# Performance work log

Hardware: AMD Instinct MI355X
Metric: run time of the kernel (lower is better)

Reference implementation:

```python
import jax, jax.numpy as jnp
from jax import lax
import numpy as np

FSIZE = 5
NUM_FILTERS = 8


def setup_inputs() -> dict:
    key = jax.random.key(0)
    k1, k2, k3 = jax.random.split(key, 3)
    B, H, W = 8, 1024, 1024
    scale = 1.0 / (FSIZE * FSIZE)  # matches .normal_(0, 1/(fsize*fsize))
    return {
        "mosaick": jax.random.uniform(k1, (B, 1, H, W), dtype=jnp.float32),
        "sel_filts": jax.random.normal(k2, (NUM_FILTERS, FSIZE, FSIZE), dtype=jnp.float32) * scale,
        "green_filts": jax.random.normal(k3, (NUM_FILTERS, FSIZE, FSIZE), dtype=jnp.float32) * scale,
    }


def _conv_bank(x_padded, filts):
    # x_padded: [B,1,H+2p,W+2p], filts: [K,f,f] -> [B,K,H,W]
    return lax.conv_general_dilated(
        x_padded, filts[:, None, :, :], (1, 1), "VALID",
        dimension_numbers=("NCHW", "OIHW", "NCHW"))


def reference(mosaick, sel_filts, green_filts):
    # Space-variant learned demosaicking of the green channel:
    # per-pixel softmax over a bank of selection-filter responses picks a
    # convex combination of candidate green interpolations; known green
    # samples (GRBG: x%2 == y%2) are passed through from the mosaick.
    B, _, H, W = mosaick.shape
    p = FSIZE // 2
    padded = jnp.pad(mosaick, ((0, 0), (0, 0), (p, p), (p, p)), mode="edge")
    sel = _conv_bank(padded, sel_filts)        # [B,K,H,W] selection scores
    interp = _conv_bank(padded, green_filts)   # [B,K,H,W] green candidates
    w = jax.nn.softmax(sel, axis=1)            # per-pixel filter weights
    green_hat = jnp.sum(w * interp, axis=1, keepdims=True)  # [B,1,H,W]
    yy = jnp.arange(H)[:, None]
    xx = jnp.arange(W)[None, :]
    gmask = ((xx % 2) == (yy % 2)).astype(mosaick.dtype)  # GRBG green sites
    green = gmask * mosaick + (1.0 - gmask) * green_hat
    return green  # corresponds to output[:, 1:2, ...]
```

## Files before the change

### kernel.cpp

```cpp
#include <hip/hip_runtime.h>

#define HH 1024
#define WW 1024

__global__ __launch_bounds__(256, 2)
void demosaick_kernel(const float* __restrict__ mosaick,
                      const float* __restrict__ sel_filts,
                      const float* __restrict__ green_filts,
                      float* __restrict__ out, int HW) {
    __shared__ float filt[25][16];

    const int tid = threadIdx.y * 64 + threadIdx.x;
    for (int idx = tid; idx < 400; idx += 256) {
        int half = idx / 200;
        int j = idx - half * 200;
        int k = j / 25;
        int t = j - k * 25;
        filt[t][half * 8 + k] = half ? green_filts[j] : sel_filts[j];
    }
    __syncthreads();

    const int b  = blockIdx.z;
    const int y0 = blockIdx.y * 16 + threadIdx.y * 4;
    const int x0 = (blockIdx.x * 64 + threadIdx.x) * 2;
    const float* img = mosaick + (size_t)b * HW;

    float win[8][6];
    #pragma unroll
    for (int j = 0; j < 8; ++j) {
        int r = y0 + j - 2;
        r = r < 0 ? 0 : (r > HH - 1 ? HH - 1 : r);
        const float* rp = img + r * WW;
        #pragma unroll
        for (int i = 0; i < 6; ++i) {
            int c = x0 + i - 2;
            c = c < 0 ? 0 : (c > WW - 1 ? WW - 1 : c);
            win[j][i] = rp[c];
        }
    }

    float aS[4][8];
    float aG[4][8];
    #pragma unroll
    for (int p = 0; p < 4; ++p)
        #pragma unroll
        for (int k = 0; k < 8; ++k) { aS[p][k] = 0.f; aG[p][k] = 0.f; }

    const float4* fl4 = (const float4*)&filt[0][0];
    #pragma unroll
    for (int dy = 0; dy < 5; ++dy) {
        #pragma unroll
        for (int dx = 0; dx < 5; ++dx) {
            const int t = dy * 5 + dx;
            float fS[8], fG[8];
            *(float4*)&fS[0] = fl4[t * 4 + 0];
            *(float4*)&fS[4] = fl4[t * 4 + 1];
            *(float4*)&fG[0] = fl4[t * 4 + 2];
            *(float4*)&fG[4] = fl4[t * 4 + 3];
            #pragma unroll
            for (int p = 0; p < 4; ++p) {
                float v = win[p + dy][dx + ((p & 1) ^ 1)];
                #pragma unroll
                for (int k = 0; k < 8; ++k) {
                    aS[p][k] = fmaf(v, fS[k], aS[p][k]);
                    aG[p][k] = fmaf(v, fG[k], aG[p][k]);
                }
            }
        }
    }

    float* outp = out + (size_t)b * HW;
    #pragma unroll
    for (int p = 0; p < 4; ++p) {
        float m = aS[p][0];
        #pragma unroll
        for (int k = 1; k < 8; ++k) m = fmaxf(m, aS[p][k]);
        float s = 0.f, gh = 0.f;
        #pragma unroll
        for (int k = 0; k < 8; ++k) {
            float e = __expf(aS[p][k] - m);
            s += e;
            gh = fmaf(e, aG[p][k], gh);
        }
        gh /= s;
        float2 o;
        if ((p & 1) == 0) { o.x = win[p + 2][2]; o.y = gh; }
        else              { o.x = gh;            o.y = win[p + 2][3]; }
        *(float2*)(outp + (size_t)(y0 + p) * WW + x0) = o;
    }
}

extern "C" void kernel_launch(void* const* d_in, const int* in_sizes, int n_in,
                              void* d_out, int out_size, void* d_ws, size_t ws_size,
                              hipStream_t stream) {
    const float* mosaick     = (const float*)d_in[0];
    const float* sel_filts   = (const float*)d_in[1];
    const float* green_filts = (const float*)d_in[2];
    float* out = (float*)d_out;
    const int HW = HH * WW;
    const int B = in_sizes[0] / HW;
    dim3 grid(WW / 128, HH / 16, B);
    dim3 block(64, 4, 1);
    hipLaunchKernelGGL(demosaick_kernel, grid, block, 0, stream,
                       mosaick, sel_filts, green_filts, out, HW);
}
```

Baseline: 126.3 us.

## Use packed FMA for filter accumulation, vector interior loads, fast reciprocal

```diff
diff --git a/kernel.cpp b/kernel.cpp
--- a/kernel.cpp
+++ b/kernel.cpp
@@ -3,11 +3,13 @@
 #define HH 1024
 #define WW 1024
 
-__global__ __launch_bounds__(256, 2)
+typedef float v2 __attribute__((ext_vector_type(2)));
+
+__global__ __launch_bounds__(256, 1)
 void demosaick_kernel(const float* __restrict__ mosaick,
                       const float* __restrict__ sel_filts,
                       const float* __restrict__ green_filts,
-                      float* __restrict__ out, int HW) {
+                      float* __restrict__ out) {
     __shared__ float filt[25][16];
 
     const int tid = threadIdx.y * 64 + threadIdx.x;
@@ -23,28 +25,41 @@
     const int b  = blockIdx.z;
     const int y0 = blockIdx.y * 16 + threadIdx.y * 4;
     const int x0 = (blockIdx.x * 64 + threadIdx.x) * 2;
-    const float* img = mosaick + (size_t)b * HW;
+    const float* img = mosaick + (size_t)b * (HH * WW);
 
     float win[8][6];
-    #pragma unroll
-    for (int j = 0; j < 8; ++j) {
-        int r = y0 + j - 2;
-        r = r < 0 ? 0 : (r > HH - 1 ? HH - 1 : r);
-        const float* rp = img + r * WW;
+    const bool interior = (blockIdx.x != 0) & (blockIdx.x != gridDim.x - 1) &
+                          (blockIdx.y != 0) & (blockIdx.y != gridDim.y - 1);
+    if (interior) {
         #pragma unroll
-        for (int i = 0; i < 6; ++i) {
-            int c = x0 + i - 2;
-            c = c < 0 ? 0 : (c > WW - 1 ? WW - 1 : c);
-            win[j][i] = rp[c];
+        for (int j = 0; j < 8; ++j) {
+            const float2* rp = (const float2*)(img + (size_t)(y0 + j - 2) * WW + (x0 - 2));
+            float2 a = rp[0], c = rp[1], e = rp[2];
+            win[j][0] = a.x; win[j][1] = a.y;
+            win[j][2] = c.x; win[j][3] = c.y;
+            win[j][4] = e.x; win[j][5] = e.y;
+        }
+    } else {
+        #pragma unroll
+        for (int j = 0; j < 8; ++j) {
+            int r = y0 + j - 2;
+            r = r < 0 ? 0 : (r > HH - 1 ? HH - 1 : r);
+            const float* rp = img + (size_t)r * WW;
+            #pragma unroll
+            for (int i = 0; i < 6; ++i) {
+                int c = x0 + i - 2;
+                c = c < 0 ? 0 : (c > WW - 1 ? WW - 1 : c);
+                win[j][i] = rp[c];
+            }
         }
     }
 
-    float aS[4][8];
-    float aG[4][8];
+    v2 accS[4][4];
+    v2 accG[4][4];
     #pragma unroll
     for (int p = 0; p < 4; ++p)
         #pragma unroll
-        for (int k = 0; k < 8; ++k) { aS[p][k] = 0.f; aG[p][k] = 0.f; }
+        for (int q = 0; q < 4; ++q) { accS[p][q] = (v2)(0.f); accG[p][q] = (v2)(0.f); }
 
     const float4* fl4 = (const float4*)&filt[0][0];
     #pragma unroll
@@ -52,37 +67,46 @@
         #pragma unroll
         for (int dx = 0; dx < 5; ++dx) {
             const int t = dy * 5 + dx;
-            float fS[8], fG[8];
-            *(float4*)&fS[0] = fl4[t * 4 + 0];
-            *(float4*)&fS[4] = fl4[t * 4 + 1];
-            *(float4*)&fG[0] = fl4[t * 4 + 2];
-            *(float4*)&fG[4] = fl4[t * 4 + 3];
+            float4 s0 = fl4[t * 4 + 0], s1 = fl4[t * 4 + 1];
+            float4 g0 = fl4[t * 4 + 2], g1 = fl4[t * 4 + 3];
+            v2 fS[4], fG[4];
+            fS[0].x = s0.x; fS[0].y = s0.y; fS[1].x = s0.z; fS[1].y = s0.w;
+            fS[2].x = s1.x; fS[2].y = s1.y; fS[3].x = s1.z; fS[3].y = s1.w;
+            fG[0].x = g0.x; fG[0].y = g0.y; fG[1].x = g0.z; fG[1].y = g0.w;
+            fG[2].x = g1.x; fG[2].y = g1.y; fG[3].x = g1.z; fG[3].y = g1.w;
             #pragma unroll
             for (int p = 0; p < 4; ++p) {
                 float v = win[p + dy][dx + ((p & 1) ^ 1)];
+                v2 vv; vv.x = v; vv.y = v;
                 #pragma unroll
-                for (int k = 0; k < 8; ++k) {
-                    aS[p][k] = fmaf(v, fS[k], aS[p][k]);
-                    aG[p][k] = fmaf(v, fG[k], aG[p][k]);
+                for (int q = 0; q < 4; ++q) {
+                    accS[p][q] = __builtin_elementwise_fma(vv, fS[q], accS[p][q]);
+                    accG[p][q] = __builtin_elementwise_fma(vv, fG[q], accG[p][q]);
                 }
             }
         }
     }
 
-    float* outp = out + (size_t)b * HW;
+    float* outp = out + (size_t)b * (HH * WW);
     #pragma unroll
     for (int p = 0; p < 4; ++p) {
-        float m = aS[p][0];
+        float sc[8], gc[8];
         #pragma unroll
-        for (int k = 1; k < 8; ++k) m = fmaxf(m, aS[p][k]);
+        for (int q = 0; q < 4; ++q) {
+            sc[2 * q] = accS[p][q].x; sc[2 * q + 1] = accS[p][q].y;
+            gc[2 * q] = accG[p][q].x; gc[2 * q + 1] = accG[p][q].y;
+        }
+        float m = sc[0];
+        #pragma unroll
+        for (int k = 1; k < 8; ++k) m = fmaxf(m, sc[k]);
         float s = 0.f, gh = 0.f;
         #pragma unroll
         for (int k = 0; k < 8; ++k) {
-            float e = __expf(aS[p][k] - m);
+            float e = __expf(sc[k] - m);
             s += e;
-            gh = fmaf(e, aG[p][k], gh);
+            gh = fmaf(e, gc[k], gh);
         }
-        gh /= s;
+        gh *= __builtin_amdgcn_rcpf(s);
         float2 o;
         if ((p & 1) == 0) { o.x = win[p + 2][2]; o.y = gh; }
         else              { o.x = gh;            o.y = win[p + 2][3]; }
@@ -102,5 +126,5 @@
     dim3 grid(WW / 128, HH / 16, B);
     dim3 block(64, 4, 1);
     hipLaunchKernelGGL(demosaick_kernel, grid, block, 0, stream,
-                       mosaick, sel_filts, green_filts, out, HW);
+                       mosaick, sel_filts, green_filts, out);
 }
```

After: 187.2 us. 48.2% more time.

## Use packed fp16 dot2 for filter bank convolutions with split green pass

Applied to the files above, without the earlier changes.

```diff
diff --git a/kernel.cpp b/kernel.cpp
--- a/kernel.cpp
+++ b/kernel.cpp
@@ -3,89 +3,142 @@
 #define HH 1024
 #define WW 1024
 
+typedef __fp16 h2 __attribute__((ext_vector_type(2)));
+
 __global__ __launch_bounds__(256, 2)
 void demosaick_kernel(const float* __restrict__ mosaick,
                       const float* __restrict__ sel_filts,
                       const float* __restrict__ green_filts,
-                      float* __restrict__ out, int HW) {
-    __shared__ float filt[25][16];
+                      float* __restrict__ out) {
+    __shared__ h2 filt2[15 * 16];
 
     const int tid = threadIdx.y * 64 + threadIdx.x;
-    for (int idx = tid; idx < 400; idx += 256) {
-        int half = idx / 200;
-        int j = idx - half * 200;
-        int k = j / 25;
-        int t = j - k * 25;
-        filt[t][half * 8 + k] = half ? green_filts[j] : sel_filts[j];
+    if (tid < 240) {
+        int ch = tid & 15;
+        int t  = tid >> 4;
+        int dy = t / 3;
+        int pr = t - dy * 3;
+        int dx0 = 2 * pr;
+        const float* src = (ch < 8) ? sel_filts : green_filts;
+        int base = (ch & 7) * 25 + dy * 5 + dx0;
+        float v0 = src[base];
+        float v1 = (dx0 + 1 < 5) ? src[base + 1] : 0.f;
+        filt2[tid] = __builtin_amdgcn_cvt_pkrtz(v0, v1);
     }
     __syncthreads();
 
     const int b  = blockIdx.z;
     const int y0 = blockIdx.y * 16 + threadIdx.y * 4;
     const int x0 = (blockIdx.x * 64 + threadIdx.x) * 2;
-    const float* img = mosaick + (size_t)b * HW;
+    const float* img = mosaick + (size_t)b * (HH * WW);
 
-    float win[8][6];
+    h2 hE[8][3];
+    h2 hO[8][3];
+    float cen[4];
     #pragma unroll
     for (int j = 0; j < 8; ++j) {
         int r = y0 + j - 2;
         r = r < 0 ? 0 : (r > HH - 1 ? HH - 1 : r);
-        const float* rp = img + r * WW;
+        const float* rp = img + (size_t)r * WW;
+        float w[6];
         #pragma unroll
         for (int i = 0; i < 6; ++i) {
             int c = x0 + i - 2;
             c = c < 0 ? 0 : (c > WW - 1 ? WW - 1 : c);
-            win[j][i] = rp[c];
+            w[i] = rp[c];
         }
+        hE[j][0] = __builtin_amdgcn_cvt_pkrtz(w[0], w[1]);
+        hE[j][1] = __builtin_amdgcn_cvt_pkrtz(w[2], w[3]);
+        hE[j][2] = __builtin_amdgcn_cvt_pkrtz(w[4], 0.f);
+        hO[j][0] = __builtin_amdgcn_cvt_pkrtz(w[1], w[2]);
+        hO[j][1] = __builtin_amdgcn_cvt_pkrtz(w[3], w[4]);
+        hO[j][2] = __builtin_amdgcn_cvt_pkrtz(w[5], 0.f);
+        if (j >= 2 && j <= 5)
+            cen[j - 2] = ((j - 2) & 1) ? w[3] : w[2];
     }
 
-    float aS[4][8];
-    float aG[4][8];
+    float accS[4][8];
     #pragma unroll
     for (int p = 0; p < 4; ++p)
         #pragma unroll
-        for (int k = 0; k < 8; ++k) { aS[p][k] = 0.f; aG[p][k] = 0.f; }
+        for (int c = 0; c < 8; ++c) accS[p][c] = 0.f;
 
-    const float4* fl4 = (const float4*)&filt[0][0];
     #pragma unroll
     for (int dy = 0; dy < 5; ++dy) {
         #pragma unroll
-        for (int dx = 0; dx < 5; ++dx) {
-            const int t = dy * 5 + dx;
-            float fS[8], fG[8];
-            *(float4*)&fS[0] = fl4[t * 4 + 0];
-            *(float4*)&fS[4] = fl4[t * 4 + 1];
-            *(float4*)&fG[0] = fl4[t * 4 + 2];
-            *(float4*)&fG[4] = fl4[t * 4 + 3];
+        for (int pr = 0; pr < 3; ++pr) {
+            const h2* fp = &filt2[(dy * 3 + pr) * 16];
+            h2 f[8];
+            #pragma unroll
+            for (int c = 0; c < 8; ++c) f[c] = fp[c];
             #pragma unroll
             for (int p = 0; p < 4; ++p) {
-                float v = win[p + dy][dx + ((p & 1) ^ 1)];
+                h2 wp = (p & 1) ? hE[p + dy][pr] : hO[p + dy][pr];
                 #pragma unroll
-                for (int k = 0; k < 8; ++k) {
-                    aS[p][k] = fmaf(v, fS[k], aS[p][k]);
-                    aG[p][k] = fmaf(v, fG[k], aG[p][k]);
-                }
+                for (int c = 0; c < 8; ++c)
+                    accS[p][c] = __builtin_amdgcn_fdot2(wp, f[c], accS[p][c], false);
             }
         }
     }
 
-    float* outp = out + (size_t)b * HW;
+    const float L2E = 1.44269504f;
+    float sum[4], gh[4];
     #pragma unroll
     for (int p = 0; p < 4; ++p) {
-        float m = aS[p][0];
+        float m = accS[p][0];
         #pragma unroll
-        for (int k = 1; k < 8; ++k) m = fmaxf(m, aS[p][k]);
-        float s = 0.f, gh = 0.f;
+        for (int c = 1; c < 8; ++c) m = fmaxf(m, accS[p][c]);
+        float mL = m * L2E;
+        float s = 0.f;
         #pragma unroll
-        for (int k = 0; k < 8; ++k) {
-            float e = __expf(aS[p][k] - m);
+        for (int c = 0; c < 8; ++c) {
+            float e = __builtin_amdgcn_exp2f(fmaf(accS[p][c], L2E, -mL));
+            accS[p][c] = e;
             s += e;
-            gh = fmaf(e, aG[p][k], gh);
         }
-        gh /= s;
+        sum[p] = s;
+        gh[p] = 0.f;
+    }
+
+    #pragma unroll
+    for (int hlf = 0; hlf < 2; ++hlf) {
+        float accG[4][4];
+        #pragma unroll
+        for (int p = 0; p < 4; ++p)
+            #pragma unroll
+            for (int c = 0; c < 4; ++c) accG[p][c] = 0.f;
+
+        #pragma unroll
+        for (int dy = 0; dy < 5; ++dy) {
+            #pragma unroll
+            for (int pr = 0; pr < 3; ++pr) {
+                const h2* fp = &filt2[(dy * 3 + pr) * 16 + 8 + 4 * hlf];
+                h2 f[4];
+                #pragma unroll
+                for (int c = 0; c < 4; ++c) f[c] = fp[c];
+                #pragma unroll
+                for (int p = 0; p < 4; ++p) {
+                    h2 wp = (p & 1) ? hE[p + dy][pr] : hO[p + dy][pr];
+                    #pragma unroll
+                    for (int c = 0; c < 4; ++c)
+                        accG[p][c] = __builtin_amdgcn_fdot2(wp, f[c], accG[p][c], false);
+                }
+            }
+        }
+        #pragma unroll
+        for (int p = 0; p < 4; ++p)
+            #pragma unroll
+            for (int c = 0; c < 4; ++c)
+                gh[p] = fmaf(accS[p][4 * hlf + c], accG[p][c], gh[p]);
+    }
+
+    float* outp = out + (size_t)b * (HH * WW);
+    #pragma unroll
+    for (int p = 0; p < 4; ++p) {
+        float g = gh[p] * __builtin_amdgcn_rcpf(sum[p]);
         float2 o;
-        if ((p & 1) == 0) { o.x = win[p + 2][2]; o.y = gh; }
-        else              { o.x = gh;            o.y = win[p + 2][3]; }
+        if ((p & 1) == 0) { o.x = cen[p]; o.y = g; }
+        else              { o.x = g;      o.y = cen[p]; }
         *(float2*)(outp + (size_t)(y0 + p) * WW + x0) = o;
     }
 }
@@ -102,5 +155,5 @@
     dim3 grid(WW / 128, HH / 16, B);
     dim3 block(64, 4, 1);
     hipLaunchKernelGGL(demosaick_kernel, grid, block, 0, stream,
-                       mosaick, sel_filts, green_filts, out, HW);
+                       mosaick, sel_filts, green_filts, out);
 }
```

Result: faster. 119.2 us (-5.6%).

## Compute filter-bank convolution with fp16 MFMA over shared-memory tiles

Applied to the files above, without the earlier changes.

```diff
diff --git a/kernel.cpp b/kernel.cpp
--- a/kernel.cpp
+++ b/kernel.cpp
@@ -1,92 +1,92 @@
 #include <hip/hip_runtime.h>
 
-#define HH 1024
-#define WW 1024
+#define HW_ (1024 * 1024)
+
+typedef _Float16 half8 __attribute__((ext_vector_type(8)));
+typedef float f32x4 __attribute__((ext_vector_type(4)));
 
 __global__ __launch_bounds__(256, 2)
-void demosaick_kernel(const float* __restrict__ mosaick,
-                      const float* __restrict__ sel_filts,
-                      const float* __restrict__ green_filts,
-                      float* __restrict__ out, int HW) {
-    __shared__ float filt[25][16];
+void demosaick_mfma(const float* __restrict__ mosaick,
+                    const float* __restrict__ sel_filts,
+                    const float* __restrict__ green_filts,
+                    float* __restrict__ out) {
+    __shared__ __align__(16) _Float16 smem[2240];
 
-    const int tid = threadIdx.y * 64 + threadIdx.x;
-    for (int idx = tid; idx < 400; idx += 256) {
-        int half = idx / 200;
-        int j = idx - half * 200;
-        int k = j / 25;
-        int t = j - k * 25;
-        filt[t][half * 8 + k] = half ? green_filts[j] : sel_filts[j];
+    const int tid = threadIdx.x;
+    const int b   = blockIdx.z;
+    const int by0 = blockIdx.y * 32, bx0 = blockIdx.x * 32;
+    const float* img = mosaick + (size_t)b * HW_;
+
+    for (int idx = tid; idx < 1440; idx += 256) {
+        int row = idx / 40, col = idx - row * 40;
+        int gy = by0 - 2 + row; gy = gy < 0 ? 0 : (gy > 1023 ? 1023 : gy);
+        int gx = bx0 - 2 + col; gx = gx < 0 ? 0 : (gx > 1023 ? 1023 : gx);
+        smem[idx] = (_Float16)img[gy * 1024 + gx];
     }
+    for (int idx = tid; idx < 512; idx += 256) {
+        int ch = idx >> 5, t = idx & 31;
+        float v = 0.f;
+        if (t < 25) v = (ch < 8) ? sel_filts[ch * 25 + t]
+                                 : green_filts[(ch - 8) * 25 + t];
+        smem[1440 + idx] = (_Float16)v;
+    }
+    for (int idx = tid; idx < 288; idx += 256)
+        smem[1952 + idx] = (_Float16)0.f;
     __syncthreads();
 
-    const int b  = blockIdx.z;
-    const int y0 = blockIdx.y * 16 + threadIdx.y * 4;
-    const int x0 = (blockIdx.x * 64 + threadIdx.x) * 2;
-    const float* img = mosaick + (size_t)b * HW;
+    const int lane = tid & 63, w = tid >> 6;
+    const int c = lane & 15, q = lane >> 4;
 
-    float win[8][6];
+    const half8 b8 = *(const half8*)&smem[1440 + c * 32 + q * 8];
+
+    int a_idx[8];
     #pragma unroll
     for (int j = 0; j < 8; ++j) {
-        int r = y0 + j - 2;
-        r = r < 0 ? 0 : (r > HH - 1 ? HH - 1 : r);
-        const float* rp = img + r * WW;
-        #pragma unroll
-        for (int i = 0; i < 6; ++i) {
-            int c = x0 + i - 2;
-            c = c < 0 ? 0 : (c > WW - 1 ? WW - 1 : c);
-            win[j][i] = rp[c];
-        }
+        int t = q * 8 + j;
+        int dy = t / 5, dx = t - dy * 5;
+        a_idx[j] = (t >= 25) ? 1952 : (w * 320 + dy * 40 + 2 * c + dx);
     }
 
-    float aS[4][8];
-    float aG[4][8];
+    float* outp = out + (size_t)b * HW_;
+    const float L2E = 1.44269504f;
+
     #pragma unroll
-    for (int p = 0; p < 4; ++p)
+    for (int g = 0; g < 8; ++g) {
+        const int imm = g * 40 + ((g & 1) ? 0 : 1);
+
+        half8 a8;
         #pragma unroll
-        for (int k = 0; k < 8; ++k) { aS[p][k] = 0.f; aG[p][k] = 0.f; }
+        for (int j = 0; j < 8; ++j) a8[j] = smem[a_idx[j] + imm];
 
-    const float4* fl4 = (const float4*)&filt[0][0];
-    #pragma unroll
-    for (int dy = 0; dy < 5; ++dy) {
+        f32x4 z = {0.f, 0.f, 0.f, 0.f};
+        f32x4 acc = __builtin_amdgcn_mfma_f32_16x16x32_f16(a8, b8, z, 0, 0, 0);
+
+        float gh[4];
         #pragma unroll
-        for (int dx = 0; dx < 5; ++dx) {
-            const int t = dy * 5 + dx;
-            float fS[8], fG[8];
-            *(float4*)&fS[0] = fl4[t * 4 + 0];
-            *(float4*)&fS[4] = fl4[t * 4 + 1];
-            *(float4*)&fG[0] = fl4[t * 4 + 2];
-            *(float4*)&fG[4] = fl4[t * 4 + 3];
-            #pragma unroll
-            for (int p = 0; p < 4; ++p) {
-                float v = win[p + dy][dx + ((p & 1) ^ 1)];
-                #pragma unroll
-                for (int k = 0; k < 8; ++k) {
-                    aS[p][k] = fmaf(v, fS[k], aS[p][k]);
-                    aG[p][k] = fmaf(v, fG[k], aG[p][k]);
-                }
-            }
+        for (int r = 0; r < 4; ++r) {
+            float own = acc[r];
+            float oth = __shfl_xor(own, 8);
+            float t0  = (c < 8) ? own : oth;
+            float e   = __builtin_amdgcn_exp2f(t0 * L2E);
+            float v   = (c < 8) ? e * oth : e;
+            v += __shfl_xor(v, 1);
+            v += __shfl_xor(v, 2);
+            v += __shfl_xor(v, 4);
+            float sums = __shfl_xor(v, 8);
+            gh[r] = v * __builtin_amdgcn_rcpf(sums);
         }
-    }
 
-    float* outp = out + (size_t)b * HW;
-    #pragma unroll
-    for (int p = 0; p < 4; ++p) {
-        float m = aS[p][0];
-        #pragma unroll
-        for (int k = 1; k < 8; ++k) m = fmaxf(m, aS[p][k]);
-        float s = 0.f, gh = 0.f;
-        #pragma unroll
-        for (int k = 0; k < 8; ++k) {
-            float e = __expf(aS[p][k] - m);
-            s += e;
-            gh = fmaf(e, aG[p][k], gh);
+        if (c < 4) {
+            int p = q * 4 + c;
+            float gv = (c == 0) ? gh[0] : (c == 1) ? gh[1]
+                     : (c == 2) ? gh[2] : gh[3];
+            float pass = (float)smem[(w * 8 + g + 2) * 40 + 2 * p + 2 + (g & 1)];
+            float2 o;
+            if (g & 1) { o.x = gv;   o.y = pass; }
+            else       { o.x = pass; o.y = gv;   }
+            int y = by0 + w * 8 + g;
+            *(float2*)(outp + (size_t)y * 1024 + bx0 + 2 * p) = o;
         }
-        gh /= s;
-        float2 o;
-        if ((p & 1) == 0) { o.x = win[p + 2][2]; o.y = gh; }
-        else              { o.x = gh;            o.y = win[p + 2][3]; }
-        *(float2*)(outp + (size_t)(y0 + p) * WW + x0) = o;
     }
 }
 
@@ -97,10 +97,9 @@
     const float* sel_filts   = (const float*)d_in[1];
     const float* green_filts = (const float*)d_in[2];
     float* out = (float*)d_out;
-    const int HW = HH * WW;
-    const int B = in_sizes[0] / HW;
-    dim3 grid(WW / 128, HH / 16, B);
-    dim3 block(64, 4, 1);
-    hipLaunchKernelGGL(demosaick_kernel, grid, block, 0, stream,
-                       mosaick, sel_filts, green_filts, out, HW);
+    const int B = in_sizes[0] / HW_;
+    dim3 grid(1024 / 32, 1024 / 32, B);
+    dim3 block(256, 1, 1);
+    hipLaunchKernelGGL(demosaick_mfma, grid, block, 0, stream,
+                       mosaick, sel_filts, green_filts, out);
 }
```

New measurement: 145.5 us. 15.2% more time.
